# Performance work log

Measured on AMD Instinct MI355X. Metric: run time of the kernel, lower is better.

Reference implementation:

```python
import jax, jax.numpy as jnp
import numpy as np

B, S, D = 1, 2048, 2048
H, KVH, HD = 32, 8, 64
FFN = 8192
N_EXPERTS, TOP_K = 32, 4
EPS = 1e-5
NEG = -1e9


def setup_inputs() -> dict:
    key = jax.random.key(0)
    ks = jax.random.split(key, 24)
    s = 0.02
    inp = {}
    inp['hidden_states'] = jax.random.normal(ks[0], (B, S, D), jnp.float32)
    # RoPE tables: cos/sin of shape [B, S, HD]
    inv_freq = 1.0 / (10000.0 ** (np.arange(0, HD, 2, dtype=np.float32) / HD))
    t = np.arange(S, dtype=np.float32)
    freqs = np.outer(t, inv_freq)                      # [S, HD/2]
    emb = np.concatenate([freqs, freqs], axis=-1)      # [S, HD]
    inp['cos'] = jnp.asarray(np.cos(emb))[None].repeat(B, axis=0)
    inp['sin'] = jnp.asarray(np.sin(emb))[None].repeat(B, axis=0)
    # additive causal mask [B, 1, S, S]
    causal = jnp.where(jnp.tril(jnp.ones((S, S), bool)), 0.0, NEG).astype(jnp.float32)
    inp['attention_mask'] = jnp.broadcast_to(causal[None, None], (B, 1, S, S))
    # attention params
    inp['wq'] = jax.random.normal(ks[1], (H * HD, D), jnp.float32) * s
    inp['bq'] = jnp.zeros((H * HD,), jnp.float32)
    inp['wk'] = jax.random.normal(ks[2], (KVH * HD, D), jnp.float32) * s
    inp['bk'] = jnp.zeros((KVH * HD,), jnp.float32)
    inp['wv'] = jax.random.normal(ks[3], (KVH * HD, D), jnp.float32) * s
    inp['bv'] = jnp.zeros((KVH * HD,), jnp.float32)
    inp['wo'] = jax.random.normal(ks[4], (D, H * HD), jnp.float32) * s
    inp['bo'] = jnp.zeros((D,), jnp.float32)
    # norms
    inp['ln1_w'] = jnp.ones((D,), jnp.float32)
    inp['ln2_w'] = jnp.ones((D,), jnp.float32)
    # MoE gate + shared expert MLP
    inp['gate_w'] = jax.random.normal(ks[5], (N_EXPERTS, D), jnp.float32) * s
    inp['gate_b'] = jnp.zeros((N_EXPERTS,), jnp.float32)
    inp['w1'] = jax.random.normal(ks[6], (FFN, D), jnp.float32) * s
    inp['b1'] = jnp.zeros((FFN,), jnp.float32)
    inp['w2'] = jax.random.normal(ks[7], (D, FFN), jnp.float32) * s
    inp['b2'] = jnp.zeros((D,), jnp.float32)
    inp['w3'] = jax.random.normal(ks[8], (FFN, D), jnp.float32) * s
    inp['b3'] = jnp.zeros((FFN,), jnp.float32)
    return inp


def _rms_norm(x, w, eps=EPS):
    x32 = x.astype(jnp.float32)
    var = jnp.mean(x32 * x32, axis=-1, keepdims=True)
    return (w * (x32 * jax.lax.rsqrt(var + eps))).astype(x.dtype)


def _rotate_half(x):
    x1, x2 = jnp.split(x, 2, axis=-1)
    return jnp.concatenate([-x2, x1], axis=-1)


def _decoder_layer(hidden_states, cos, sin, attention_mask,
                   wq, bq, wk, bk, wv, bv, wo, bo, ln1_w, ln2_w,
                   gate_w, gate_b, w1, b1, w2, b2, w3, b3):
    residual = hidden_states
    x = _rms_norm(hidden_states, ln1_w)

    # projections -> [B, heads, S, HD]
    q = (x @ wq.T + bq).reshape(B, S, H, HD).transpose(0, 2, 1, 3)
    k = (x @ wk.T + bk).reshape(B, S, KVH, HD).transpose(0, 2, 1, 3)
    v = (x @ wv.T + bv).reshape(B, S, KVH, HD).transpose(0, 2, 1, 3)

    # RoPE (cos/sin unsqueezed on head dim)
    c, s_ = cos[:, None], sin[:, None]
    q = q * c + _rotate_half(q) * s_
    k = k * c + _rotate_half(k) * s_

    # GQA: repeat kv heads
    n_rep = H // KVH
    k = jnp.repeat(k, n_rep, axis=1)
    v = jnp.repeat(v, n_rep, axis=1)

    scaling = HD ** -0.5
    scores = jnp.einsum('bhqd,bhkd->bhqk', q, k) * scaling + attention_mask
    probs = jax.nn.softmax(scores.astype(jnp.float32), axis=-1).astype(q.dtype)
    attn = jnp.einsum('bhqk,bhkd->bhqd', probs, v)
    attn = attn.transpose(0, 2, 1, 3).reshape(B, S, H * HD)
    attn = attn @ wo.T + bo

    hidden_states = residual + attn
    residual = hidden_states
    x = _rms_norm(hidden_states, ln2_w)

    # MoE block (as written in source: router computed, but ALL tokens go
    # through one shared expert MLP; routing weights unused in output)
    flat = x.reshape(-1, D)
    router_logits = flat @ gate_w.T + gate_b                     # [B*S, E]
    rw = jax.nn.softmax(router_logits.astype(jnp.float32), axis=-1)
    rw_top, sel = jax.lax.top_k(rw, TOP_K)                       # computed, unused
    del rw_top, sel

    h1 = flat @ w1.T + b1
    h3 = flat @ w3.T + b3
    mlp = (jax.nn.silu(h1) * h3) @ w2.T + b2
    hidden_states = residual + mlp.reshape(B, S, D)
    return hidden_states


def reference(hidden_states, cos, sin, attention_mask,
              wq, bq, wk, bk, wv, bv, wo, bo, ln1_w, ln2_w,
              gate_w, gate_b, w1, b1, w2, b2, w3, b3):
    return _decoder_layer(hidden_states, cos, sin, attention_mask,
                          wq, bq, wk, bk, wv, bv, wo, bo, ln1_w, ln2_w,
                          gate_w, gate_b, w1, b1, w2, b2, w3, b3)
```

## Files before the change

kernel.cpp:

```cpp
#include <hip/hip_runtime.h>

#define S_LEN 2048
#define DMODEL 2048
#define NH 32
#define NKV 8
#define HD 64
#define FFN_DIM 8192

typedef __attribute__((ext_vector_type(4))) float f32x4;
typedef __attribute__((ext_vector_type(16))) float f32x16;
typedef __attribute__((ext_vector_type(8))) short bf16x8;

#define MFMA(a, b, c) __builtin_amdgcn_mfma_f32_16x16x32_bf16(a, b, c, 0, 0, 0)
#define MFMA32(a, b, c) __builtin_amdgcn_mfma_f32_32x32x16_bf16(a, b, c, 0, 0, 0)

__device__ __forceinline__ ushort f2bf(float f) {
  unsigned u = __float_as_uint(f);
  unsigned r = (u + 0x7fffu + ((u >> 16) & 1u)) >> 16;
  return (ushort)r;
}
__device__ __forceinline__ float bf2f(ushort s) {
  return __uint_as_float(((unsigned)s) << 16);
}
__device__ __forceinline__ unsigned cvtpk(float a, float b) {
  unsigned r;
  asm("v_cvt_pk_bf16_f32 %0, %1, %2" : "=v"(r) : "v"(a), "v"(b));
  return r;
}

__device__ __forceinline__ void gload16(const void* g, void* l) {
  __builtin_amdgcn_global_load_lds(
      (const __attribute__((address_space(1))) void*)g,
      (__attribute__((address_space(3))) void*)l, 16, 0, 0);
}

__device__ __forceinline__ void cvt_row8(const float* src, ushort* dst,
                                         int i) {
  f32x4 a = *(const f32x4*)(src + i);
  f32x4 b = *(const f32x4*)(src + i + 4);
  bf16x8 r;
#pragma unroll
  for (int j = 0; j < 4; j++) r[j] = (short)f2bf(a[j]);
#pragma unroll
  for (int j = 0; j < 4; j++) r[4 + j] = (short)f2bf(b[j]);
  *(bf16x8*)(dst + i) = r;
}

__global__ __launch_bounds__(256) void cvt_k(const float* __restrict__ in,
                                             ushort* __restrict__ out) {
  int i = blockIdx.x * 256 + threadIdx.x;
  f32x4 a = ((const f32x4*)in)[i * 2];
  f32x4 b = ((const f32x4*)in)[i * 2 + 1];
  bf16x8 r;
#pragma unroll
  for (int j = 0; j < 4; j++) r[j] = (short)f2bf(a[j]);
#pragma unroll
  for (int j = 0; j < 4; j++) r[4 + j] = (short)f2bf(b[j]);
  ((bf16x8*)out)[i] = r;
}

__global__ __launch_bounds__(256) void cvt_qkv_k(const float* __restrict__ wq,
                                                 const float* __restrict__ wk,
                                                 const float* __restrict__ wv,
                                                 ushort* __restrict__ dst) {
  int row = blockIdx.x;
  const float* src;
  if (row < 2048) src = wq + (size_t)row * DMODEL;
  else if (row < 2560) src = wk + (size_t)(row - 2048) * DMODEL;
  else src = wv + (size_t)(row - 2560) * DMODEL;
  cvt_row8(src, dst + (size_t)row * DMODEL, threadIdx.x * 8);
}

__global__ __launch_bounds__(256) void cvt_w13_k(const float* __restrict__ w1,
                                                 const float* __restrict__ w3,
                                                 ushort* __restrict__ dst) {
  int r = blockIdx.x;
  int nb = r >> 8, i5 = r & 255;
  int wn = i5 >> 6, nf = (i5 >> 4) & 3, e = i5 & 15;
  int L = nb * 128 + wn * 32 + (nf >> 1) * 16 + e;
  const float* src = ((nf & 1) ? w3 : w1) + (size_t)L * DMODEL;
  cvt_row8(src, dst + (size_t)r * DMODEL, threadIdx.x * 8);
}

__global__ __launch_bounds__(256) void bias3_k(const float* __restrict__ a,
                                               const float* __restrict__ b,
                                               const float* __restrict__ c,
                                               float* __restrict__ out) {
  int i = blockIdx.x * 256 + threadIdx.x;
  float v;
  if (i < 2048) v = a[i];
  else if (i < 2560) v = b[i - 2048];
  else v = c[i - 2560];
  out[i] = v;
}

__global__ __launch_bounds__(256) void rmsnorm_k(const float* __restrict__ in,
                                                 const float* __restrict__ w,
                                                 ushort* __restrict__ out) {
  const int row = blockIdx.x;
  const int tid = threadIdx.x;
  const float* x = in + (size_t)row * DMODEL;
  f32x4 v0 = *(const f32x4*)(x + tid * 8);
  f32x4 v1 = *(const f32x4*)(x + tid * 8 + 4);
  float ss = v0[0] * v0[0] + v0[1] * v0[1] + v0[2] * v0[2] + v0[3] * v0[3] +
             v1[0] * v1[0] + v1[1] * v1[1] + v1[2] * v1[2] + v1[3] * v1[3];
#pragma unroll
  for (int off = 32; off; off >>= 1) ss += __shfl_xor(ss, off, 64);
  __shared__ float red[4];
  if ((tid & 63) == 0) red[tid >> 6] = ss;
  __syncthreads();
  float tot = red[0] + red[1] + red[2] + red[3];
  float inv = rsqrtf(tot * (1.f / DMODEL) + 1e-5f);
#pragma unroll
  for (int i = 0; i < 8; i++) {
    int c = tid * 8 + i;
    float val = (i < 4) ? v0[i] : v1[i - 4];
    out[(size_t)row * DMODEL + c] = f2bf(w[c] * val * inv);
  }
}

enum { EPI_PART = 0, EPI_SILU2 = 1 };

#define QUAD(AS, BS, MROW, NCOL)                                     \
  _Pragma("unroll") for (int kk_ = 0; kk_ < 2; kk_++)                \
  _Pragma("unroll") for (int mf_ = 0; mf_ < 4; mf_++)                \
  _Pragma("unroll") for (int nf_ = 0; nf_ < 2; nf_++)                \
      acc[(MROW) + mf_][(NCOL) + nf_] =                              \
          MFMA(AS[2 * mf_ + kk_], BS[2 * nf_ + kk_],                 \
               acc[(MROW) + mf_][(NCOL) + nf_]);

#define PHASE_MID                                    \
  __builtin_amdgcn_sched_barrier(0);                 \
  __builtin_amdgcn_s_barrier();                      \
  asm volatile("s_waitcnt lgkmcnt(0)" ::: "memory"); \
  __builtin_amdgcn_sched_barrier(0);                 \
  __builtin_amdgcn_s_setprio(1);

#define PHASE_CLOSE                                  \
  __builtin_amdgcn_s_setprio(0);                     \
  __builtin_amdgcn_sched_barrier(0);                 \
  __builtin_amdgcn_s_barrier();

#define RD_A(PA0, PA1, J0)                           \
  _Pragma("unroll") for (int j_ = 0; j_ < 4; j_++) { \
    A_[2 * j_] = *(const bf16x8*)((PA0) + ((J0) + j_) * 1024);     \
    A_[2 * j_ + 1] = *(const bf16x8*)((PA1) + ((J0) + j_) * 1024); \
  }
#define RD_B(DST, PB0, PB1, J0)                      \
  _Pragma("unroll") for (int n_ = 0; n_ < 2; n_++) { \
    DST[2 * n_] = *(const bf16x8*)((PB0) + ((J0) + n_) * 1024);     \
    DST[2 * n_ + 1] = *(const bf16x8*)((PB1) + ((J0) + n_) * 1024); \
  }

template <int EPI>
__global__ __launch_bounds__(512, 2) void gemm256(
    const ushort* __restrict__ A, int lda, const ushort* __restrict__ B,
    int ldb, const float* __restrict__ b1v, const float* __restrict__ b3v,
    ushort* __restrict__ outb, int ldc, int K, int kspan, long long opart) {
  __shared__ __align__(16) ushort lds[65536];
  const int tid = threadIdx.x;
  const int l = tid & 63, w = tid >> 6;
  const int g = l >> 4, r16 = l & 15;
  const int wm = w >> 2, wn = w & 3;

  int nwg = gridDim.x * gridDim.y;
  int bid = blockIdx.y * gridDim.x + blockIdx.x;
  bid = (bid & 7) * (nwg >> 3) + (bid >> 3);
  const int m0 = (bid % gridDim.x) * 256;
  const int n0 = (bid / gridDim.x) * 256;
  const int z = blockIdx.z;

  const ushort* Ag = A + (size_t)z * kspan + (size_t)m0 * lda;
  const ushort* Bg = B + (size_t)z * kspan + (size_t)n0 * ldb;
  ushort* outbz = outb + (size_t)z * opart;

  const int NT = K >> 6, NI = NT >> 1;

  const int stgRow = w * 8 + (l >> 3);
  const int stgCol = ((l & 7) ^ (l >> 3)) * 8;

  const int xa = (r16 & 7) << 4;
  const int c0 = ((g * 16) ^ xa) >> 1;
  const int c1 = c0 ^ 32;
  const int aslot = wm ? 24576 : 8192;
  const int bslot = ((wn >> 1) ? 16384 : 0) + (wn & 1) * 4096;
  const ushort* pA0b0 = lds + aslot + r16 * 64 + c0;
  const ushort* pA1b0 = lds + aslot + r16 * 64 + c1;
  const ushort* pA0b1 = pA0b0 + 32768;
  const ushort* pA1b1 = pA1b0 + 32768;
  const ushort* pB0b0 = lds + bslot + r16 * 64 + c0;
  const ushort* pB1b0 = lds + bslot + r16 * 64 + c1;
  const ushort* pB0b1 = pB0b0 + 32768;
  const ushort* pB1b1 = pB1b0 + 32768;

  f32x4 acc[8][4];
#pragma unroll
  for (int i = 0; i < 8; i++)
#pragma unroll
    for (int j = 0; j < 4; j++) acc[i][j] = (f32x4){0, 0, 0, 0};

  auto stageA = [&](int slot, int tile, int hf) {
    ushort* dst = lds + ((tile & 1) * 32768 + slot * 8192 + w * 512);
    const ushort* src =
        Ag + (size_t)(hf * 128 + stgRow) * lda + tile * 64 + stgCol;
    gload16(src, dst);
    gload16(src + (size_t)64 * lda, dst + 4096);
  };
  auto stageB = [&](int slot, int tile, int hf) {
    ushort* dst = lds + ((tile & 1) * 32768 + slot * 8192 + w * 512);
    const ushort* src =
        Bg + (size_t)(hf * 128 + stgRow) * ldb + tile * 64 + stgCol;
    gload16(src, dst);
    gload16(src + (size_t)64 * ldb, dst + 4096);
  };

  stageB(0, 0, 0);
  stageB(2, 0, 1);
  stageA(1, 0, 0);
  stageA(3, 0, 1);
  stageB(0, 1, 0);
  stageB(2, 1, 1);
  asm volatile("s_waitcnt vmcnt(4)" ::: "memory");
  __builtin_amdgcn_s_barrier();

  bf16x8 A_[8], Blo[4], Bhi[4];

  for (int i = 0; i < NI; ++i) {
    const int ta = 2 * i, tb = 2 * i + 1;
    const bool st = (ta + 2 < NT);
    RD_A(pA0b0, pA1b0, 0);
    RD_B(Blo, pB0b0, pB1b0, 0);
    stageA(1, tb, 0);
    asm volatile("s_waitcnt lgkmcnt(8)" ::: "memory");
    PHASE_MID; QUAD(A_, Blo, 0, 0); PHASE_CLOSE;
    RD_B(Bhi, pB0b0, pB1b0, 2);
    stageA(3, tb, 1);
    PHASE_MID; QUAD(A_, Bhi, 0, 2); PHASE_CLOSE;
    RD_A(pA0b0, pA1b0, 4);
    if (st) stageB(0, ta + 2, 0);
    PHASE_MID; QUAD(A_, Bhi, 4, 2); PHASE_CLOSE;
    if (st) stageB(2, ta + 2, 1);
    PHASE_MID; QUAD(A_, Blo, 4, 0);
    __builtin_amdgcn_s_setprio(0);
    __builtin_amdgcn_sched_barrier(0);
    if (st) {
      asm volatile("s_waitcnt vmcnt(4)" ::: "memory");
    } else {
      asm volatile("s_waitcnt vmcnt(0)" ::: "memory");
    }
    __builtin_amdgcn_s_barrier();
    RD_A(pA0b1, pA1b1, 0);
    RD_B(Blo, pB0b1, pB1b1, 0);
    if (st) stageA(1, ta + 2, 0);
    asm volatile("s_waitcnt lgkmcnt(8)" ::: "memory");
    PHASE_MID; QUAD(A_, Blo, 0, 0); PHASE_CLOSE;
    RD_B(Bhi, pB0b1, pB1b1, 2);
    if (st) stageA(3, ta + 2, 1);
    PHASE_MID; QUAD(A_, Bhi, 0, 2); PHASE_CLOSE;
    RD_A(pA0b1, pA1b1, 4);
    if (st) stageB(0, tb + 2, 0);
    PHASE_MID; QUAD(A_, Bhi, 4, 2); PHASE_CLOSE;
    if (st) stageB(2, tb + 2, 1);
    PHASE_MID; QUAD(A_, Blo, 4, 0);
    __builtin_amdgcn_s_setprio(0);
    __builtin_amdgcn_sched_barrier(0);
    asm volatile("s_waitcnt vmcnt(4)" ::: "memory");
    __builtin_amdgcn_s_barrier();
  }

  if constexpr (EPI == EPI_PART) {
#pragma unroll
    for (int mf = 0; mf < 8; mf++)
#pragma unroll
      for (int nf = 0; nf < 4; nf++) {
        const int n = n0 + wn * 64 + nf * 16 + r16;
#pragma unroll
        for (int reg = 0; reg < 4; reg++) {
          const int m = m0 + wm * 128 + mf * 16 + g * 4 + reg;
          outbz[(size_t)m * ldc + n] = f2bf(acc[mf][nf][reg]);
        }
      }
  } else {
#pragma unroll
    for (int mf = 0; mf < 8; mf++)
#pragma unroll
      for (int p = 0; p < 2; p++) {
        const int L = (n0 >> 1) + wn * 32 + p * 16 + r16;
        const float bb1 = b1v[L], bb3 = b3v[L];
#pragma unroll
        for (int reg = 0; reg < 4; reg++) {
          const int m = m0 + wm * 128 + mf * 16 + g * 4 + reg;
          float h1 = acc[mf][2 * p][reg] + bb1;
          float h3 = acc[mf][2 * p + 1][reg] + bb3;
          float sv = h1 / (1.f + __expf(-h1));
          outbz[(size_t)m * ldc + L] = f2bf(sv * h3);
        }
      }
  }
}

__global__ __launch_bounds__(384) void reduceQ_rope_k(
    const ushort* __restrict__ part, const float* __restrict__ bias,
    const float* __restrict__ cs, const float* __restrict__ sn,
    ushort* __restrict__ qkv) {
  __shared__ float row[3072];
  const int r = blockIdx.x;
  const int col = threadIdx.x * 8;
  const long long ps = (long long)S_LEN * 3072;
  float s[8];
#pragma unroll
  for (int j = 0; j < 8; j++) s[j] = bias[col + j];
#pragma unroll
  for (int z = 0; z < 2; z++) {
    bf16x8 v = *(const bf16x8*)(part + z * ps + (size_t)r * 3072 + col);
#pragma unroll
    for (int j = 0; j < 8; j++) s[j] += bf2f((ushort)v[j]);
  }
#pragma unroll
  for (int j = 0; j < 8; j++) row[col + j] = s[j];
  __syncthreads();
  ushort o[8];
  if (col < 2560) {
    const float* c = cs + r * HD + (col & 63);
    const float* si = sn + r * HD + (col & 63);
    const float sgn = (col & 32) ? 1.f : -1.f;
    const int pc = col ^ 32;
#pragma unroll
    for (int j = 0; j < 8; j++)
      o[j] = f2bf(s[j] * c[j] + sgn * row[pc + j] * si[j]);
  } else {
#pragma unroll
    for (int j = 0; j < 8; j++) o[j] = f2bf(s[j]);
  }
  bf16x8 rr;
#pragma unroll
  for (int j = 0; j < 8; j++) rr[j] = (short)o[j];
  *(bf16x8*)(qkv + (size_t)r * 3072 + col) = rr;
}

__global__ __launch_bounds__(256) void reduceO_rms_k(
    const ushort* __restrict__ part, const float* __restrict__ bias,
    const float* __restrict__ resid, const float* __restrict__ lnw,
    float* __restrict__ outf, ushort* __restrict__ x2) {
  const int r = blockIdx.x;
  const int tid = threadIdx.x;
  const int col = tid * 8;
  const long long ps = (long long)S_LEN * DMODEL;
  float s[8];
#pragma unroll
  for (int j = 0; j < 8; j++) s[j] = bias[col + j] + resid[(size_t)r * DMODEL + col + j];
#pragma unroll
  for (int z = 0; z < 4; z++) {
    bf16x8 v = *(const bf16x8*)(part + z * ps + (size_t)r * DMODEL + col);
#pragma unroll
    for (int j = 0; j < 8; j++) s[j] += bf2f((ushort)v[j]);
  }
  float ss = 0.f;
#pragma unroll
  for (int j = 0; j < 8; j++) ss += s[j] * s[j];
#pragma unroll
  for (int off = 32; off; off >>= 1) ss += __shfl_xor(ss, off, 64);
  __shared__ float red[4];
  if ((tid & 63) == 0) red[tid >> 6] = ss;
  f32x4 o0, o1;
#pragma unroll
  for (int j = 0; j < 4; j++) { o0[j] = s[j]; o1[j] = s[4 + j]; }
  *(f32x4*)(outf + (size_t)r * DMODEL + col) = o0;
  *(f32x4*)(outf + (size_t)r * DMODEL + col + 4) = o1;
  __syncthreads();
  float tot = red[0] + red[1] + red[2] + red[3];
  float inv = rsqrtf(tot * (1.f / DMODEL) + 1e-5f);
  bf16x8 rr;
#pragma unroll
  for (int j = 0; j < 8; j++) rr[j] = (short)f2bf(lnw[col + j] * s[j] * inv);
  *(bf16x8*)(x2 + (size_t)r * DMODEL + col) = rr;
}

__global__ __launch_bounds__(256) void reduceW_k(
    const ushort* __restrict__ part, const float* __restrict__ bias,
    float* __restrict__ out) {
  long long i = (long long)(blockIdx.x * 256 + threadIdx.x) * 8;
  int col = (int)(i % DMODEL);
  const long long ps = (long long)S_LEN * DMODEL;
  float s[8];
#pragma unroll
  for (int j = 0; j < 8; j++) s[j] = bias[col + j] + out[i + j];
#pragma unroll
  for (int z = 0; z < 4; z++) {
    bf16x8 v = *(const bf16x8*)(part + z * ps + i);
#pragma unroll
    for (int j = 0; j < 8; j++) s[j] += bf2f((ushort)v[j]);
  }
#pragma unroll
  for (int j = 0; j < 8; j++) out[i + j] = s[j];
}

__global__ __launch_bounds__(256, 3) void flash2_k(
    const ushort* __restrict__ qkv, ushort* __restrict__ att, int nFlash,
    int nCvtTasks, const float* __restrict__ wo, const float* __restrict__ w1,
    const float* __restrict__ w3, const float* __restrict__ w2s,
    ushort* __restrict__ cwA, ushort* __restrict__ cwB) {
  if ((int)blockIdx.x >= nFlash) {
    const int cb = blockIdx.x - nFlash;
    const int NC = gridDim.x - nFlash;
    const int i = threadIdx.x * 8;
    for (int t = cb; t < nCvtTasks; t += NC) {
      const float* src;
      ushort* dst;
      if (t < 2048) {
        src = wo + (size_t)t * DMODEL;
        dst = cwB + (size_t)t * DMODEL;
      } else if (t < 18432) {
        int r = t - 2048;
        int nb = r >> 8, i5 = r & 255;
        int wn = i5 >> 6, nf = (i5 >> 4) & 3, e = i5 & 15;
        int L = nb * 128 + wn * 32 + (nf >> 1) * 16 + e;
        src = ((nf & 1) ? w3 : w1) + (size_t)L * DMODEL;
        dst = cwA + (size_t)r * DMODEL;
      } else {
        int r = t - 18432;
        src = w2s + (size_t)r * 2048;
        dst = cwB + (size_t)2048 * DMODEL + (size_t)r * 2048;
      }
      cvt_row8(src, dst, i);
    }
    return;
  }
  const int bid = blockIdx.x;
  const int head = (bid >> 4) & 31;
  const int rmap = bid & 15;
  const int qb = (bid & 256) ? (15 - rmap) : rmap;
  const int kvh = head >> 2;
  const int tid = threadIdx.x;
  const int w = tid >> 6, l = tid & 63;
  const int h = l >> 5, q31 = l & 31;
  const int qw = qb * 128 + w * 32;
  const int qrow = qw + q31;

  __shared__ __align__(16) ushort lds[2][8192];

  bf16x8 qreg[4];
  {
    const ushort* qp = qkv + (size_t)qrow * 3072 + head * HD;
#pragma unroll
    for (int s = 0; s < 4; s++)
      qreg[s] = *(const bf16x8*)(qp + s * 16 + h * 8);
  }

  f32x16 oacc[2];
#pragma unroll
  for (int i = 0; i < 16; i++) { oacc[0][i] = 0.f; oacc[1][i] = 0.f; }
  float mreg = -1e30f, lsum = 0.f;

  const int nt = 2 * qb + 2;

  const int skv = tid >> 2;
  const int sch = (tid & 3) * 2;
  const int vkv = tid & 63;
  const int vd0 = (tid >> 6) * 16;

  const ushort* kg_base = qkv + DMODEL + kvh * HD;

  bf16x8 krA, krB, vrA, vrB;
  auto loadTile = [&](int jb) {
    const ushort* kg = kg_base + (size_t)jb * 64 * 3072;
    krA = *(const bf16x8*)(kg + (size_t)skv * 3072 + sch * 8);
    krB = *(const bf16x8*)(kg + (size_t)skv * 3072 + sch * 8 + 8);
    const ushort* vg = kg + 512;
    vrA = *(const bf16x8*)(vg + (size_t)vkv * 3072 + vd0);
    vrB = *(const bf16x8*)(vg + (size_t)vkv * 3072 + vd0 + 8);
  };
  auto writeTile = [&](int b) {
    ushort* kb = lds[b];
    *(bf16x8*)(kb + skv * 64 + ((sch ^ (skv & 7)) * 8)) = krA;
    *(bf16x8*)(kb + skv * 64 + (((sch + 1) ^ (skv & 7)) * 8)) = krB;
    ushort* vb = lds[b] + 4096;
#pragma unroll
    for (int i = 0; i < 8; i++) {
      int d = vd0 + i;
      vb[d * 64 + (((vkv >> 3) ^ (d & 7)) * 8) + (vkv & 7)] = (ushort)vrA[i];
    }
#pragma unroll
    for (int i = 0; i < 8; i++) {
      int d = vd0 + 8 + i;
      vb[d * 64 + (((vkv >> 3) ^ (d & 7)) * 8) + (vkv & 7)] = (ushort)vrB[i];
    }
  };

  loadTile(0);
  for (int jb = 0; jb < nt; ++jb) {
    const int b = jb & 1;
    writeTile(b);
    __syncthreads();
    if (jb + 1 < nt) loadTile(jb + 1);

    if (jb * 64 <= qw + 31) {
      const ushort* Kb = lds[b];
      const ushort* Vb = lds[b] + 4096;

      f32x16 sacc[2];
#pragma unroll
      for (int i = 0; i < 16; i++) { sacc[0][i] = 0.f; sacc[1][i] = 0.f; }
#pragma unroll
      for (int c = 0; c < 2; c++) {
        const int kvr = c * 32 + q31;
        const ushort* kp = Kb + kvr * 64;
        const int kx = kvr & 7;
#pragma unroll
        for (int s = 0; s < 4; s++) {
          bf16x8 kf = *(const bf16x8*)(kp + ((2 * s + h) ^ kx) * 8);
          sacc[c] = MFMA32(kf, qreg[s], sacc[c]);
        }
      }

      const bool diag = (jb * 64 + 63 > qw);
      if (diag) {
#pragma unroll
        for (int c = 0; c < 2; c++)
#pragma unroll
          for (int rg = 0; rg < 16; rg++) {
            int kvg = jb * 64 + c * 32 + (rg & 3) + 8 * (rg >> 2) + 4 * h;
            if (kvg > qrow) sacc[c][rg] = -1e30f;
          }
      }
      float tmax = sacc[0][0];
#pragma unroll
      for (int rg = 1; rg < 16; rg++) tmax = fmaxf(tmax, sacc[0][rg]);
#pragma unroll
      for (int rg = 0; rg < 16; rg++) tmax = fmaxf(tmax, sacc[1][rg]);
      tmax = fmaxf(tmax, __shfl_xor(tmax, 32));
      const float mn = fmaxf(mreg, tmax);
      const float resc = __expf((mreg - mn) * 0.125f);
      mreg = mn;
      float rsum = 0.f;
#pragma unroll
      for (int c = 0; c < 2; c++)
#pragma unroll
        for (int rg = 0; rg < 16; rg++) {
          float pv = __expf((sacc[c][rg] - mn) * 0.125f);
          sacc[c][rg] = pv;
          rsum += pv;
        }
      rsum += __shfl_xor(rsum, 32);
      lsum = lsum * resc + rsum;
      oacc[0] *= resc;
      oacc[1] *= resc;

      unsigned pw_[2][4][2];
#pragma unroll
      for (int c = 0; c < 2; c++)
#pragma unroll
        for (int rr = 0; rr < 4; rr++) {
          pw_[c][rr][0] = cvtpk(sacc[c][4 * rr + 0], sacc[c][4 * rr + 1]);
          pw_[c][rr][1] = cvtpk(sacc[c][4 * rr + 2], sacc[c][4 * rr + 3]);
        }

#pragma unroll
      for (int s = 0; s < 4; s++) {
        const int c = s >> 1, base = (s & 1) * 2;
        unsigned k0 = h ? pw_[c][base + 1][0] : pw_[c][base][0];
        unsigned k1 = h ? pw_[c][base + 1][1] : pw_[c][base][1];
        unsigned s0 = h ? pw_[c][base][0] : pw_[c][base + 1][0];
        unsigned s1 = h ? pw_[c][base][1] : pw_[c][base + 1][1];
        unsigned t0 = __shfl_xor(s0, 32);
        unsigned t1 = __shfl_xor(s1, 32);
        union { unsigned u[4]; bf16x8 v; } pf;
        pf.u[0] = h ? t0 : k0;
        pf.u[1] = h ? t1 : k1;
        pf.u[2] = h ? k0 : t0;
        pf.u[3] = h ? k1 : t1;
#pragma unroll
        for (int dt = 0; dt < 2; dt++) {
          const int d = dt * 32 + q31;
          bf16x8 vf =
              *(const bf16x8*)(Vb + d * 64 + ((2 * s + h) ^ (d & 7)) * 8);
          oacc[dt] = MFMA32(vf, pf.v, oacc[dt]);
        }
      }
    }
  }

  const float inv = 1.f / lsum;
  ushort* op = att + (size_t)qrow * DMODEL + head * HD;
#pragma unroll
  for (int dt = 0; dt < 2; dt++)
#pragma unroll
    for (int rr = 0; rr < 4; rr++) {
      const int d0 = dt * 32 + 8 * rr + 4 * h;
      unsigned lo = cvtpk(oacc[dt][4 * rr + 0] * inv, oacc[dt][4 * rr + 1] * inv);
      unsigned hi = cvtpk(oacc[dt][4 * rr + 2] * inv, oacc[dt][4 * rr + 3] * inv);
      uint2 v2;
      v2.x = lo;
      v2.y = hi;
      *(uint2*)(op + d0) = v2;
    }
}

extern "C" void kernel_launch(void* const* d_in, const int* in_sizes, int n_in,
                              void* d_out, int out_size, void* d_ws,
                              size_t ws_size, hipStream_t stream) {
  (void)in_sizes; (void)n_in; (void)out_size;
  const float* hidden = (const float*)d_in[0];
  const float* cosb = (const float*)d_in[1];
  const float* sinb = (const float*)d_in[2];
  const float* wq = (const float*)d_in[4];
  const float* bq = (const float*)d_in[5];
  const float* wk = (const float*)d_in[6];
  const float* bk = (const float*)d_in[7];
  const float* wv = (const float*)d_in[8];
  const float* bv = (const float*)d_in[9];
  const float* wo = (const float*)d_in[10];
  const float* bo = (const float*)d_in[11];
  const float* ln1 = (const float*)d_in[12];
  const float* ln2 = (const float*)d_in[13];
  const float* w1 = (const float*)d_in[16];
  const float* b1 = (const float*)d_in[17];
  const float* w2 = (const float*)d_in[18];
  const float* b2 = (const float*)d_in[19];
  const float* w3 = (const float*)d_in[20];
  const float* b3 = (const float*)d_in[21];
  float* out = (float*)d_out;

  char* base = (char*)d_ws;
  char* ws = base;
  ushort* x1 = (ushort*)ws;   ws += (size_t)S_LEN * DMODEL * 2;
  ushort* qkv = (ushort*)ws;  ws += (size_t)S_LEN * 3072 * 2;
  ushort* att = (ushort*)ws;  ws += (size_t)S_LEN * DMODEL * 2;
  ushort* x2 = (ushort*)ws;   ws += (size_t)S_LEN * DMODEL * 2;
  ushort* hbuf = (ushort*)ws; ws += (size_t)S_LEN * FFN_DIM * 2;
  ushort* cwA = (ushort*)ws;  ws += (size_t)2 * FFN_DIM * DMODEL * 2;
  float* bqkv = (float*)ws;   ws += 4096 * 4;
  ushort* cwB = (ushort*)ws;
  const size_t cwB_bytes = (size_t)(2048 + 8192) * DMODEL * 2;
  const bool bigws = ((size_t)(ws - base) + cwB_bytes) <= ws_size;

  ushort* partQ = att;
  ushort* partO = hbuf;
  ushort* partW = x1;

  rmsnorm_k<<<S_LEN, 256, 0, stream>>>(hidden, ln1, x1);

  cvt_qkv_k<<<3072, 256, 0, stream>>>(wq, wk, wv, cwA);
  bias3_k<<<12, 256, 0, stream>>>(bq, bk, bv, bqkv);

  gemm256<EPI_PART><<<dim3(8, 12, 2), 512, 0, stream>>>(
      x1, DMODEL, cwA, DMODEL, nullptr, nullptr, partQ, 3072, 1024, 1024,
      (long long)S_LEN * 3072);
  reduceQ_rope_k<<<S_LEN, 384, 0, stream>>>(partQ, bqkv, cosb, sinb, qkv);

  const ushort *Bo, *B13, *B2;
  if (bigws) {
    flash2_k<<<512 + 256, 256, 0, stream>>>(qkv, att, 512, 26624, wo, w1, w3,
                                            w2, cwA, cwB);
    Bo = cwB;
    B13 = cwA;
    B2 = cwB + (size_t)2048 * DMODEL;
  } else {
    flash2_k<<<512, 256, 0, stream>>>(qkv, att, 512, 0, wo, w1, w3, w2, cwA,
                                      cwA);
    Bo = cwA;
    B13 = cwA;
    B2 = cwA;
  }

  if (!bigws) cvt_k<<<(2048 * 2048) / 2048, 256, 0, stream>>>(wo, (ushort*)Bo);
  gemm256<EPI_PART><<<dim3(8, 8, 4), 512, 0, stream>>>(
      att, DMODEL, Bo, DMODEL, nullptr, nullptr, partO, DMODEL, 512, 512,
      (long long)S_LEN * DMODEL);
  reduceO_rms_k<<<S_LEN, 256, 0, stream>>>(partO, bo, hidden, ln2, out, x2);

  if (!bigws) cvt_w13_k<<<2 * FFN_DIM, 256, 0, stream>>>(w1, w3, (ushort*)B13);
  gemm256<EPI_SILU2><<<dim3(8, 64), 512, 0, stream>>>(
      x2, DMODEL, B13, DMODEL, b1, b3, hbuf, FFN_DIM, DMODEL, 0, 0);

  if (!bigws) cvt_k<<<(DMODEL * FFN_DIM) / 2048, 256, 0, stream>>>(w2, (ushort*)B2);
  gemm256<EPI_PART><<<dim3(8, 8, 4), 512, 0, stream>>>(
      hbuf, FFN_DIM, B2, FFN_DIM, nullptr, nullptr, partW, DMODEL, 2048, 2048,
      (long long)S_LEN * DMODEL);
  reduceW_k<<<(S_LEN * DMODEL) / 2048, 256, 0, stream>>>(partW, b2, out);
}
```

Before: 378.4 us.

## Fuse prologue kernels and halve flash attention block size to 128 threads

Merges the rmsnorm, QKV weight conversion and bias concat kernels into one launch to cut launch overhead. Flash attention moves to 128-thread blocks covering 64 query rows each, doubling the grid to 1024 attention blocks plus 512 conversion blocks. Each thread now loads four K/V chunks per tile, and conversion threads handle two 8-element chunks per row. This aims for better load balance across the causal triangle and more resident blocks, at the cost of reloading each K/V tile for twice as many query blocks.

```diff
diff --git a/kernel.cpp b/kernel.cpp
--- a/kernel.cpp
+++ b/kernel.cpp
@@ -46,6 +46,51 @@
   *(bf16x8*)(dst + i) = r;
 }
 
+__global__ __launch_bounds__(256) void pre_k(
+    const float* __restrict__ hidden, const float* __restrict__ ln1,
+    ushort* __restrict__ x1, const float* __restrict__ wq,
+    const float* __restrict__ wk, const float* __restrict__ wv,
+    ushort* __restrict__ cw, const float* __restrict__ bq,
+    const float* __restrict__ bk, const float* __restrict__ bv,
+    float* __restrict__ bqkv) {
+  const int b = blockIdx.x;
+  const int tid = threadIdx.x;
+  if (b < 2048) {
+    const float* x = hidden + (size_t)b * DMODEL;
+    f32x4 v0 = *(const f32x4*)(x + tid * 8);
+    f32x4 v1 = *(const f32x4*)(x + tid * 8 + 4);
+    float ss = v0[0] * v0[0] + v0[1] * v0[1] + v0[2] * v0[2] + v0[3] * v0[3] +
+               v1[0] * v1[0] + v1[1] * v1[1] + v1[2] * v1[2] + v1[3] * v1[3];
+#pragma unroll
+    for (int off = 32; off; off >>= 1) ss += __shfl_xor(ss, off, 64);
+    __shared__ float red[4];
+    if ((tid & 63) == 0) red[tid >> 6] = ss;
+    __syncthreads();
+    float tot = red[0] + red[1] + red[2] + red[3];
+    float inv = rsqrtf(tot * (1.f / DMODEL) + 1e-5f);
+#pragma unroll
+    for (int i = 0; i < 8; i++) {
+      int c = tid * 8 + i;
+      float val = (i < 4) ? v0[i] : v1[i - 4];
+      x1[(size_t)b * DMODEL + c] = f2bf(ln1[c] * val * inv);
+    }
+  } else if (b < 5120) {
+    int row = b - 2048;
+    const float* src;
+    if (row < 2048) src = wq + (size_t)row * DMODEL;
+    else if (row < 2560) src = wk + (size_t)(row - 2048) * DMODEL;
+    else src = wv + (size_t)(row - 2560) * DMODEL;
+    cvt_row8(src, cw + (size_t)row * DMODEL, tid * 8);
+  } else {
+    int i = (b - 5120) * 256 + tid;
+    float v;
+    if (i < 2048) v = bq[i];
+    else if (i < 2560) v = bk[i - 2048];
+    else v = bv[i - 2560];
+    bqkv[i] = v;
+  }
+}
+
 __global__ __launch_bounds__(256) void cvt_k(const float* __restrict__ in,
                                              ushort* __restrict__ out) {
   int i = blockIdx.x * 256 + threadIdx.x;
@@ -57,18 +102,6 @@
 #pragma unroll
   for (int j = 0; j < 4; j++) r[4 + j] = (short)f2bf(b[j]);
   ((bf16x8*)out)[i] = r;
-}
-
-__global__ __launch_bounds__(256) void cvt_qkv_k(const float* __restrict__ wq,
-                                                 const float* __restrict__ wk,
-                                                 const float* __restrict__ wv,
-                                                 ushort* __restrict__ dst) {
-  int row = blockIdx.x;
-  const float* src;
-  if (row < 2048) src = wq + (size_t)row * DMODEL;
-  else if (row < 2560) src = wk + (size_t)(row - 2048) * DMODEL;
-  else src = wv + (size_t)(row - 2560) * DMODEL;
-  cvt_row8(src, dst + (size_t)row * DMODEL, threadIdx.x * 8);
 }
 
 __global__ __launch_bounds__(256) void cvt_w13_k(const float* __restrict__ w1,
@@ -80,43 +113,6 @@
   int L = nb * 128 + wn * 32 + (nf >> 1) * 16 + e;
   const float* src = ((nf & 1) ? w3 : w1) + (size_t)L * DMODEL;
   cvt_row8(src, dst + (size_t)r * DMODEL, threadIdx.x * 8);
-}
-
-__global__ __launch_bounds__(256) void bias3_k(const float* __restrict__ a,
-                                               const float* __restrict__ b,
-                                               const float* __restrict__ c,
-                                               float* __restrict__ out) {
-  int i = blockIdx.x * 256 + threadIdx.x;
-  float v;
-  if (i < 2048) v = a[i];
-  else if (i < 2560) v = b[i - 2048];
-  else v = c[i - 2560];
-  out[i] = v;
-}
-
-__global__ __launch_bounds__(256) void rmsnorm_k(const float* __restrict__ in,
-                                                 const float* __restrict__ w,
-                                                 ushort* __restrict__ out) {
-  const int row = blockIdx.x;
-  const int tid = threadIdx.x;
-  const float* x = in + (size_t)row * DMODEL;
-  f32x4 v0 = *(const f32x4*)(x + tid * 8);
-  f32x4 v1 = *(const f32x4*)(x + tid * 8 + 4);
-  float ss = v0[0] * v0[0] + v0[1] * v0[1] + v0[2] * v0[2] + v0[3] * v0[3] +
-             v1[0] * v1[0] + v1[1] * v1[1] + v1[2] * v1[2] + v1[3] * v1[3];
-#pragma unroll
-  for (int off = 32; off; off >>= 1) ss += __shfl_xor(ss, off, 64);
-  __shared__ float red[4];
-  if ((tid & 63) == 0) red[tid >> 6] = ss;
-  __syncthreads();
-  float tot = red[0] + red[1] + red[2] + red[3];
-  float inv = rsqrtf(tot * (1.f / DMODEL) + 1e-5f);
-#pragma unroll
-  for (int i = 0; i < 8; i++) {
-    int c = tid * 8 + i;
-    float val = (i < 4) ? v0[i] : v1[i - 4];
-    out[(size_t)row * DMODEL + c] = f2bf(w[c] * val * inv);
-  }
 }
 
 enum { EPI_PART = 0, EPI_SILU2 = 1 };
@@ -395,7 +391,7 @@
   for (int j = 0; j < 8; j++) out[i + j] = s[j];
 }
 
-__global__ __launch_bounds__(256, 3) void flash2_k(
+__global__ __launch_bounds__(128, 3) void flash2_k(
     const ushort* __restrict__ qkv, ushort* __restrict__ att, int nFlash,
     int nCvtTasks, const float* __restrict__ wo, const float* __restrict__ w1,
     const float* __restrict__ w3, const float* __restrict__ w2s,
@@ -423,18 +419,19 @@
         dst = cwB + (size_t)2048 * DMODEL + (size_t)r * 2048;
       }
       cvt_row8(src, dst, i);
+      cvt_row8(src, dst, i + 1024);
     }
     return;
   }
   const int bid = blockIdx.x;
-  const int head = (bid >> 4) & 31;
-  const int rmap = bid & 15;
-  const int qb = (bid & 256) ? (15 - rmap) : rmap;
+  const int head = (bid >> 5) & 31;
+  const int rmap = bid & 31;
+  const int qb = (bid & 512) ? (31 - rmap) : rmap;
   const int kvh = head >> 2;
   const int tid = threadIdx.x;
   const int w = tid >> 6, l = tid & 63;
   const int h = l >> 5, q31 = l & 31;
-  const int qw = qb * 128 + w * 32;
+  const int qw = qb * 64 + w * 32;
   const int qrow = qw + q31;
 
   __shared__ __align__(16) ushort lds[2][8192];
@@ -452,39 +449,39 @@
   for (int i = 0; i < 16; i++) { oacc[0][i] = 0.f; oacc[1][i] = 0.f; }
   float mreg = -1e30f, lsum = 0.f;
 
-  const int nt = 2 * qb + 2;
-
-  const int skv = tid >> 2;
-  const int sch = (tid & 3) * 2;
+  const int nt = qb + 1;
+
+  const int skv = tid >> 1;
+  const int sc4 = (tid & 1) * 4;
   const int vkv = tid & 63;
-  const int vd0 = (tid >> 6) * 16;
+  const int vd0 = (tid >> 6) * 32;
 
   const ushort* kg_base = qkv + DMODEL + kvh * HD;
 
-  bf16x8 krA, krB, vrA, vrB;
+  bf16x8 kr[4], vr[4];
   auto loadTile = [&](int jb) {
     const ushort* kg = kg_base + (size_t)jb * 64 * 3072;
-    krA = *(const bf16x8*)(kg + (size_t)skv * 3072 + sch * 8);
-    krB = *(const bf16x8*)(kg + (size_t)skv * 3072 + sch * 8 + 8);
+#pragma unroll
+    for (int c = 0; c < 4; c++)
+      kr[c] = *(const bf16x8*)(kg + (size_t)skv * 3072 + (sc4 + c) * 8);
     const ushort* vg = kg + 512;
-    vrA = *(const bf16x8*)(vg + (size_t)vkv * 3072 + vd0);
-    vrB = *(const bf16x8*)(vg + (size_t)vkv * 3072 + vd0 + 8);
+#pragma unroll
+    for (int c = 0; c < 4; c++)
+      vr[c] = *(const bf16x8*)(vg + (size_t)vkv * 3072 + vd0 + c * 8);
   };
   auto writeTile = [&](int b) {
     ushort* kb = lds[b];
-    *(bf16x8*)(kb + skv * 64 + ((sch ^ (skv & 7)) * 8)) = krA;
-    *(bf16x8*)(kb + skv * 64 + (((sch + 1) ^ (skv & 7)) * 8)) = krB;
+#pragma unroll
+    for (int c = 0; c < 4; c++)
+      *(bf16x8*)(kb + skv * 64 + (((sc4 + c) ^ (skv & 7)) * 8)) = kr[c];
     ushort* vb = lds[b] + 4096;
 #pragma unroll
-    for (int i = 0; i < 8; i++) {
-      int d = vd0 + i;
-      vb[d * 64 + (((vkv >> 3) ^ (d & 7)) * 8) + (vkv & 7)] = (ushort)vrA[i];
-    }
-#pragma unroll
-    for (int i = 0; i < 8; i++) {
-      int d = vd0 + 8 + i;
-      vb[d * 64 + (((vkv >> 3) ^ (d & 7)) * 8) + (vkv & 7)] = (ushort)vrB[i];
-    }
+    for (int c = 0; c < 4; c++)
+#pragma unroll
+      for (int i = 0; i < 8; i++) {
+        int d = vd0 + c * 8 + i;
+        vb[d * 64 + (((vkv >> 3) ^ (d & 7)) * 8) + (vkv & 7)] = (ushort)vr[c][i];
+      }
   };
 
   loadTile(0);
@@ -638,10 +635,8 @@
   ushort* partO = hbuf;
   ushort* partW = x1;
 
-  rmsnorm_k<<<S_LEN, 256, 0, stream>>>(hidden, ln1, x1);
-
-  cvt_qkv_k<<<3072, 256, 0, stream>>>(wq, wk, wv, cwA);
-  bias3_k<<<12, 256, 0, stream>>>(bq, bk, bv, bqkv);
+  pre_k<<<5132, 256, 0, stream>>>(hidden, ln1, x1, wq, wk, wv, cwA, bq, bk, bv,
+                                  bqkv);
 
   gemm256<EPI_PART><<<dim3(8, 12, 2), 512, 0, stream>>>(
       x1, DMODEL, cwA, DMODEL, nullptr, nullptr, partQ, 3072, 1024, 1024,
@@ -650,14 +645,14 @@
 
   const ushort *Bo, *B13, *B2;
   if (bigws) {
-    flash2_k<<<512 + 256, 256, 0, stream>>>(qkv, att, 512, 26624, wo, w1, w3,
-                                            w2, cwA, cwB);
+    flash2_k<<<1024 + 512, 128, 0, stream>>>(qkv, att, 1024, 26624, wo, w1, w3,
+                                             w2, cwA, cwB);
     Bo = cwB;
     B13 = cwA;
     B2 = cwB + (size_t)2048 * DMODEL;
   } else {
-    flash2_k<<<512, 256, 0, stream>>>(qkv, att, 512, 0, wo, w1, w3, w2, cwA,
-                                      cwA);
+    flash2_k<<<1024, 128, 0, stream>>>(qkv, att, 1024, 0, wo, w1, w3, w2, cwA,
+                                       cwA);
     Bo = cwA;
     B13 = cwA;
     B2 = cwA;
```

Result: no change. 377.0 us, median of 2 (-0.4%).
